# Optimization experiments

Hardware: AMD Instinct MI355X
Metric: run time of the kernel (lower is better)

Reference implementation:

```python
import jax, jax.numpy as jnp
import numpy as np

EMBED = 256
PC_RANGE = np.array([-51.2, -51.2, -5.0, 51.2, 51.2, 3.0], np.float32)
INF_PC_RANGE = np.array([0.0, -51.2, -5.0, 102.4, 51.2, 3.0], np.float32)
EPS = 1e-5
NUM_THINGS = 3
THRESHOLD = 0.05


def _inverse_sigmoid(x):
    # mmdet inverse_sigmoid with eps=1e-5
    x = jnp.clip(x, 0.0, 1.0)
    x1 = jnp.clip(x, EPS, None)
    x2 = jnp.clip(1.0 - x, EPS, None)
    return jnp.log(x1 / x2)


def _norm2lidar(locs, pc_range):
    lo = jnp.asarray(pc_range[:3])
    hi = jnp.asarray(pc_range[3:])
    return locs * (hi - lo) + lo


def _lidar2norm(locs, pc_range):
    lo = jnp.asarray(pc_range[:3])
    hi = jnp.asarray(pc_range[3:])
    return (locs - lo) / (hi - lo)


def _transform(pts, calib):
    # pts [..., 3]; homogeneous transform with calib [4,4]
    h = jnp.concatenate([pts, jnp.ones_like(pts[..., :1])], -1)
    return jnp.einsum('ij,...j->...i', calib, h)[..., :3]


def setup_inputs() -> dict:
    key = jax.random.key(0)
    ks = jax.random.split(key, 16)
    L, BS, NI, NV, C = 6, 1, 8192, 16384, 3
    # logits shifted positive so sigmoid > 0.05 for every (query, class):
    # matching torch's duplicate-index gather semantics).
    inf_cls = jnp.abs(jax.random.normal(ks[0], (L, BS, NI, C), jnp.float32)) + 0.2
    inp = {
        'inf_outputs_classes': inf_cls,
        'inf_outputs_coords': jax.random.uniform(ks[1], (L, BS, NI, 4), jnp.float32),
        'inf_query': jax.random.normal(ks[2], (BS, NI, EMBED), jnp.float32),
        'inf_query_pos': jax.random.normal(ks[3], (BS, NI, EMBED), jnp.float32),
        'inf_reference': jax.random.normal(ks[4], (BS, NI, 4), jnp.float32),
        'veh_outputs_classes': jax.random.normal(ks[5], (L, BS, NV, C), jnp.float32),
        'veh_outputs_coords': jax.random.uniform(ks[6], (L, BS, NV, 4), jnp.float32),
        'veh_query': jax.random.normal(ks[7], (BS, NV, EMBED), jnp.float32),
        'veh_query_pos': jax.random.normal(ks[8], (BS, NV, EMBED), jnp.float32),
        'veh_reference': jax.random.normal(ks[9], (BS, NV, 4), jnp.float32),
    }
    # valid rigid inf->veh calibration T; module computes calib = inv(veh2inf_rt[0].T)
    th = 0.3
    T = np.eye(4, dtype=np.float64)
    T[:3, :3] = [[np.cos(th), -np.sin(th), 0.0], [np.sin(th), np.cos(th), 0.0], [0.0, 0.0, 1.0]]
    T[:3, 3] = [10.0, 2.0, 0.5]
    inp['veh2inf_rt'] = jnp.asarray(np.linalg.inv(T).T, jnp.float32)[None]
    s = 0.05
    inp['W_align'] = jax.random.normal(ks[10], (EMBED + 9, EMBED), jnp.float32) * s
    inp['b_align'] = jax.random.normal(ks[11], (EMBED,), jnp.float32) * s
    inp['W_align_pos'] = jax.random.normal(ks[12], (EMBED + 9, EMBED), jnp.float32) * s
    inp['b_align_pos'] = jax.random.normal(ks[13], (EMBED,), jnp.float32) * s
    return inp


def reference(inf_outputs_classes, inf_outputs_coords, inf_query, inf_query_pos,
              inf_reference, veh_outputs_classes, veh_outputs_coords, veh_query,
              veh_query_pos, veh_reference, veh2inf_rt, W_align, b_align,
              W_align_pos, b_align_pos):
    # calibration goes through numpy in the original -> constant, non-differentiable
    calib = jnp.asarray(np.linalg.inv(np.asarray(veh2inf_rt[0], np.float64).T), jnp.float32)

    # ---- filter_inf_lanes: threshold on last-layer sigmoid scores ----
    cls_score = jax.nn.sigmoid(inf_outputs_classes[-1])            # [bs, N, C]
    indexes = jnp.nonzero(cls_score.reshape(-1) > THRESHOLD)[0]
    bbox_index = indexes // NUM_THINGS                              # duplicates kept

    inf_outputs_classes = inf_outputs_classes[:, :, bbox_index, :]
    inf_outputs_coords = inf_outputs_coords[:, :, bbox_index, :]
    inf_query = inf_query[:, bbox_index, :]
    inf_query_pos = inf_query_pos[:, bbox_index, :]
    inf_reference = inf_reference[:, bbox_index, :]

    # ---- reference points: inf norm -> inf lidar -> veh lidar -> veh norm ----
    ref3 = jnp.concatenate([inf_reference[..., :2],
                            jnp.zeros_like(inf_reference[..., :1])], -1)  # [bs,N,3]
    locs = jax.nn.sigmoid(ref3)                    # _norm2lidar inverse_sigmoid mode
    locs = _norm2lidar(locs, INF_PC_RANGE)
    locs = _transform(locs, calib)
    locs = _inverse_sigmoid(_lidar2norm(locs, PC_RANGE))
    inf_reference = inf_reference.at[..., :2].set(locs[..., :2])

    # ---- per-layer bbox centers: same transform in sigmoid space ----
    bb3 = jnp.concatenate([inf_outputs_coords[..., :2],
                           jnp.zeros_like(inf_outputs_coords[..., :1])], -1)  # [L,bs,N,3]
    bb3 = _norm2lidar(bb3, INF_PC_RANGE)
    bb3 = _transform(bb3, calib)
    bb3 = _lidar2norm(bb3, PC_RANGE)
    inf_outputs_coords = inf_outputs_coords.at[..., :2].set(bb3[..., :2])

    # ---- cross-agent query alignment with rotation conditioning ----
    r = calib[:3, :3].reshape(9)
    r_b = jnp.broadcast_to(r, inf_query.shape[:-1] + (9,))
    inf_query = jnp.concatenate([inf_query, r_b], -1) @ W_align + b_align
    inf_query_pos = jnp.concatenate([inf_query_pos, r_b], -1) @ W_align_pos + b_align_pos

    # ---- complement vehicle-side sets with aligned inf lanes ----
    outputs_classes = jnp.concatenate([veh_outputs_classes, inf_outputs_classes], axis=2)
    outputs_coords = jnp.concatenate([veh_outputs_coords, inf_outputs_coords], axis=2)
    query = jnp.concatenate([veh_query, inf_query], axis=1)
    query_pos = jnp.concatenate([veh_query_pos, inf_query_pos], axis=1)
    reference = jnp.concatenate([veh_reference, inf_reference], axis=1)
    return (outputs_classes, outputs_coords, query, query_pos, reference)
```

## Files before the change

### kernel.cpp

```cpp
#include <hip/hip_runtime.h>
#include <hip/hip_bf16.h>

#define EMBED 256
#define LL 6

typedef __attribute__((ext_vector_type(8))) __bf16 bf16x8;
typedef __attribute__((ext_vector_type(4))) float f32x4;

#define SEL_THR (-2.9444389791664403f)

__global__ __launch_bounds__(1024) void k_select_calib(
        const float* __restrict__ cls, int n,
        const float* __restrict__ rt, float* __restrict__ calib,
        int* __restrict__ bbox, int* __restrict__ cnt) {
    __shared__ int warpCnt[16];
    int tid = threadIdx.x;
    int wid = tid >> 6, lane = tid & 63;

    if (tid == 0) {
        double a[4][8];
        for (int i = 0; i < 4; ++i)
            for (int j = 0; j < 4; ++j) {
                a[i][j]     = (double)rt[j * 4 + i];
                a[i][4 + j] = (i == j) ? 1.0 : 0.0;
            }
        for (int c = 0; c < 4; ++c) {
            int p = c; double best = fabs(a[c][c]);
            for (int r = c + 1; r < 4; ++r) { double v = fabs(a[r][c]); if (v > best) { best = v; p = r; } }
            if (p != c) for (int j = 0; j < 8; ++j) { double t = a[c][j]; a[c][j] = a[p][j]; a[p][j] = t; }
            double inv = 1.0 / a[c][c];
            for (int j = 0; j < 8; ++j) a[c][j] *= inv;
            for (int r = 0; r < 4; ++r) if (r != c) {
                double f = a[r][c];
                for (int j = 0; j < 8; ++j) a[r][j] -= f * a[c][j];
            }
        }
        for (int i = 0; i < 4; ++i)
            for (int j = 0; j < 4; ++j) calib[i * 4 + j] = (float)a[i][4 + j];
    }

    int PT = ((n + 1023) / 1024 + 3) & ~3;
    int PT4 = PT >> 2;
    int start = tid * PT;

    float4 v[16];
#pragma unroll
    for (int j4 = 0; j4 < 16; ++j4) {
        if (j4 < PT4) {
            int s = start + j4 * 4;
            if (s + 4 <= n) {
                v[j4] = *(const float4*)&cls[s];
            } else {
                float4 t; t.x = t.y = t.z = t.w = -1e30f;
                if (s + 0 < n) t.x = cls[s + 0];
                if (s + 1 < n) t.y = cls[s + 1];
                if (s + 2 < n) t.z = cls[s + 2];
                if (s + 3 < n) t.w = cls[s + 3];
                v[j4] = t;
            }
        }
    }
    int c = 0;
#pragma unroll
    for (int j4 = 0; j4 < 16; ++j4) {
        if (j4 < PT4) {
            c += (v[j4].x > SEL_THR) + (v[j4].y > SEL_THR) +
                 (v[j4].z > SEL_THR) + (v[j4].w > SEL_THR);
        }
    }
    int incl = c;
#pragma unroll
    for (int off = 1; off < 64; off <<= 1) {
        int u = __shfl_up(incl, off, 64);
        if (lane >= off) incl += u;
    }
    if (lane == 63) warpCnt[wid] = incl;
    __syncthreads();
    int base = 0;
    for (int w2 = 0; w2 < wid; ++w2) base += warpCnt[w2];
    int pos = base + incl - c;

#pragma unroll
    for (int j4 = 0; j4 < 16; ++j4) {
        if (j4 < PT4) {
            int s = start + j4 * 4;
            if (s + 0 < n && v[j4].x > SEL_THR) bbox[pos++] = (s + 0) / 3;
            if (s + 1 < n && v[j4].y > SEL_THR) bbox[pos++] = (s + 1) / 3;
            if (s + 2 < n && v[j4].z > SEL_THR) bbox[pos++] = (s + 2) / 3;
            if (s + 3 < n && v[j4].w > SEL_THR) bbox[pos++] = (s + 3) / 3;
        }
    }
    if (tid == 0) {
        int tot = 0;
        for (int w2 = 0; w2 < 16; ++w2) tot += warpCnt[w2];
        *cnt = tot;
    }
}

__global__ __launch_bounds__(256) void k_prep(
        const float* __restrict__ W0, const float* __restrict__ W1,
        const float* __restrict__ b0, const float* __restrict__ b1,
        const float* __restrict__ calib,
        __bf16* __restrict__ Wt0, __bf16* __restrict__ Wt1,
        float* __restrict__ bvec0, float* __restrict__ bvec1) {
    int which = blockIdx.z;
    const float* W = which ? W1 : W0;
    __bf16* Wt     = which ? Wt1 : Wt0;
    int k0 = blockIdx.x * 64, c0 = blockIdx.y * 64;
    __shared__ float T[64][65];
    int tid = threadIdx.x;
#pragma unroll
    for (int i = 0; i < 16; ++i) {
        int idx = i * 256 + tid;
        int kk = idx >> 6, cc = idx & 63;
        T[kk][cc] = W[(size_t)(k0 + kk) * EMBED + c0 + cc];
    }
    __syncthreads();
#pragma unroll
    for (int i = 0; i < 16; ++i) {
        int idx = i * 256 + tid;
        int cc = idx >> 6, kk = idx & 63;
        Wt[(size_t)(c0 + cc) * EMBED + k0 + kk] = (__bf16)T[kk][cc];
    }
    if (blockIdx.x == 0 && blockIdx.y == 0) {
        const float* b = which ? b1 : b0;
        float* o       = which ? bvec1 : bvec0;
        float s = b[tid];
#pragma unroll
        for (int u = 0; u < 9; ++u) {
            float r = calib[(u / 3) * 4 + (u % 3)];
            s += r * W[(EMBED + u) * EMBED + tid];
        }
        o[tid] = s;
    }
}

struct Plan {
    const float* src[8];
    int start[9];
    int n4[5];
    int dstOff[8];
    int perLay4[2];
    int layStride[2];
    int K, NI, NV, N;
};

__device__ __forceinline__ float inv_sig(float v) {
    v = fminf(fmaxf(v, 0.0f), 1.0f);
    float x1 = fmaxf(v, 1e-5f);
    float x2 = fmaxf(1.0f - v, 1e-5f);
    return logf(x1 / x2);
}

__global__ __launch_bounds__(256) void k_fused(Plan P, const int* __restrict__ bbox,
                                               const float* __restrict__ calib,
                                               float* __restrict__ out) {
    int bx = blockIdx.x;
    int j = 0;
    while (bx >= P.start[j + 1]) ++j;
    int lb  = bx - P.start[j];
    int tid = threadIdx.x;

    if (j < 5) {
#pragma unroll
        for (int it = 0; it < 4; ++it) {
            int i4 = lb * 1024 + it * 256 + tid;
            if (i4 < P.n4[j]) {
                float4 v = *(const float4*)&P.src[j][(size_t)i4 * 4];
                size_t d;
                if (j < 2) {
                    int l = i4 / P.perLay4[j];
                    int r = i4 - l * P.perLay4[j];
                    d = (size_t)P.dstOff[j] + (size_t)l * P.layStride[j] + (size_t)r * 4;
                } else {
                    d = (size_t)P.dstOff[j] + (size_t)i4 * 4;
                }
                *(float4*)&out[d] = v;
            }
        }
        return;
    }

    int k = lb * 256 + tid;
    if (k >= P.K) return;
    int box = bbox[k]; box = max(0, min(box, P.NI - 1));

    if (j == 5) {
        const float* s0 = P.src[5];
#pragma unroll
        for (int l = 0; l < LL; ++l) {
            const float* s = s0 + ((size_t)l * P.NI + box) * 3;
            size_t d = (size_t)P.dstOff[5] + ((size_t)l * P.N + P.NV) * 3 + (size_t)k * 3;
            out[d + 0] = s[0]; out[d + 1] = s[1]; out[d + 2] = s[2];
        }
    } else if (j == 6) {
        float c00 = calib[0], c01 = calib[1], c03 = calib[3];
        float c10 = calib[4], c11 = calib[5], c13 = calib[7];
        float zx = calib[2] * -5.0f, zy = calib[6] * -5.0f;
#pragma unroll
        for (int l = 0; l < LL; ++l) {
            float4 s = *(const float4*)&P.src[6][((size_t)l * P.NI + box) * 4];
            float X = s.x * 102.4f;
            float Y = s.y * 102.4f - 51.2f;
            float tx = c00 * X + c01 * Y + zx + c03;
            float ty = c10 * X + c11 * Y + zy + c13;
            float4 v = make_float4((tx + 51.2f) * (1.0f / 102.4f),
                                   (ty + 51.2f) * (1.0f / 102.4f), s.z, s.w);
            *(float4*)&out[(size_t)P.dstOff[6] + ((size_t)l * P.N + P.NV + k) * 4] = v;
        }
    } else {
        float4 s = *(const float4*)&P.src[7][(size_t)box * 4];
        float sx = 1.0f / (1.0f + expf(-s.x));
        float sy = 1.0f / (1.0f + expf(-s.y));
        float X = sx * 102.4f;
        float Y = sy * 102.4f - 51.2f;
        float tx = calib[0] * X + calib[1] * Y + calib[2] * -1.0f + calib[3];
        float ty = calib[4] * X + calib[5] * Y + calib[6] * -1.0f + calib[7];
        float4 v = make_float4(inv_sig((tx + 51.2f) * (1.0f / 102.4f)),
                               inv_sig((ty + 51.2f) * (1.0f / 102.4f)), s.z, s.w);
        *(float4*)&out[(size_t)P.dstOff[7] + ((size_t)P.NV + k) * 4] = v;
    }
}

__device__ __forceinline__ bf16x8 cvt8(float4 f0, float4 f1) {
    bf16x8 r;
    r[0] = (__bf16)f0.x; r[1] = (__bf16)f0.y; r[2] = (__bf16)f0.z; r[3] = (__bf16)f0.w;
    r[4] = (__bf16)f1.x; r[5] = (__bf16)f1.y; r[6] = (__bf16)f1.z; r[7] = (__bf16)f1.w;
    return r;
}

__global__ __launch_bounds__(256) void k_gemm_mfma(
        const float* __restrict__ q0, const float* __restrict__ q1,
        const int* __restrict__ bbox,
        const __bf16* __restrict__ Wt0, const __bf16* __restrict__ Wt1,
        const float* __restrict__ bvec0, const float* __restrict__ bvec1,
        float* __restrict__ out, int NI, int K, int off0, int off1) {
    int which = blockIdx.y;
    const float* q    = which ? q1 : q0;
    const __bf16* Wt  = which ? Wt1 : Wt0;
    const float* bvec = which ? bvec1 : bvec0;
    int out_off       = which ? off1 : off0;

    int tid  = threadIdx.x;
    int w    = tid >> 6;
    int lane = tid & 63;
    int lo16 = lane & 15;
    int kg   = lane >> 4;

    int r0 = blockIdx.x * 64;

    const float* aptr[4];
#pragma unroll
    for (int t = 0; t < 4; ++t) {
        int row = r0 + 16 * t + lo16;
        int rc = min(row, K - 1);
        int box = bbox[rc]; box = max(0, min(box, NI - 1));
        aptr[t] = q + (size_t)box * EMBED + kg * 8;
    }
    const __bf16* bptr[4];
#pragma unroll
    for (int t = 0; t < 4; ++t) {
        int col = w * 64 + 16 * t + lo16;
        bptr[t] = Wt + (size_t)col * EMBED + kg * 8;
    }

    f32x4 acc[4][4];
#pragma unroll
    for (int ct = 0; ct < 4; ++ct) {
        float bv = bvec[w * 64 + 16 * ct + lo16];
#pragma unroll
        for (int rt = 0; rt < 4; ++rt) {
            acc[rt][ct][0] = bv; acc[rt][ct][1] = bv; acc[rt][ct][2] = bv; acc[rt][ct][3] = bv;
        }
    }

    for (int s = 0; s < 8; ++s) {
        bf16x8 a[4], b[4];
#pragma unroll
        for (int t = 0; t < 4; ++t) {
            float4 f0 = *(const float4*)(aptr[t] + s * 32);
            float4 f1 = *(const float4*)(aptr[t] + s * 32 + 4);
            a[t] = cvt8(f0, f1);
            b[t] = *(const bf16x8*)(bptr[t] + s * 32);
        }
#pragma unroll
        for (int rt = 0; rt < 4; ++rt)
#pragma unroll
            for (int ct = 0; ct < 4; ++ct)
                acc[rt][ct] = __builtin_amdgcn_mfma_f32_16x16x32_bf16(a[rt], b[ct], acc[rt][ct], 0, 0, 0);
    }

#pragma unroll
    for (int rt = 0; rt < 4; ++rt) {
#pragma unroll
        for (int reg = 0; reg < 4; ++reg) {
            int row = r0 + 16 * rt + kg * 4 + reg;
            if (row < K) {
#pragma unroll
                for (int ct = 0; ct < 4; ++ct) {
                    int col = w * 64 + 16 * ct + lo16;
                    out[out_off + (size_t)row * EMBED + col] = acc[rt][ct][reg];
                }
            }
        }
    }
}

extern "C" void kernel_launch(void* const* d_in, const int* in_sizes, int n_in,
                              void* d_out, int out_size, void* d_ws, size_t ws_size,
                              hipStream_t stream) {
    const float* inf_cls   = (const float*)d_in[0];
    const float* inf_coord = (const float*)d_in[1];
    const float* inf_q     = (const float*)d_in[2];
    const float* inf_qp    = (const float*)d_in[3];
    const float* inf_ref   = (const float*)d_in[4];
    const float* veh_cls   = (const float*)d_in[5];
    const float* veh_coord = (const float*)d_in[6];
    const float* veh_q     = (const float*)d_in[7];
    const float* veh_qp    = (const float*)d_in[8];
    const float* veh_ref   = (const float*)d_in[9];
    const float* rt        = (const float*)d_in[10];
    const float* W0        = (const float*)d_in[11];
    const float* b0        = (const float*)d_in[12];
    const float* W1        = (const float*)d_in[13];
    const float* b1        = (const float*)d_in[14];
    float* out = (float*)d_out;

    int NI = in_sizes[0] / (LL * 3);
    int NV = in_sizes[5] / (LL * 3);
    int N  = out_size / 558;
    int K  = N - NV;

    int off_cls   = 0;
    int off_coord = LL * N * 3;
    int off_q     = off_coord + LL * N * 4;
    int off_qp    = off_q + N * EMBED;
    int off_ref   = off_qp + N * EMBED;

    char* ws = (char*)d_ws;
    float* calib = (float*)(ws);
    float* bvec0 = (float*)(ws + 128);
    float* bvec1 = (float*)(ws + 1152);
    int*   cnt   = (int*)(ws + 2176);
    int*   bbox  = (int*)(ws + 2304);
    __bf16* Wt0  = (__bf16*)(ws + 131072);
    __bf16* Wt1  = (__bf16*)(ws + 262144);

    hipLaunchKernelGGL(k_select_calib, dim3(1), dim3(1024), 0, stream,
                       inf_cls + (size_t)(LL - 1) * NI * 3, NI * 3, rt, calib, bbox, cnt);
    hipLaunchKernelGGL(k_prep, dim3(4, 4, 2), dim3(256), 0, stream,
                       W0, W1, b0, b1, calib, Wt0, Wt1, bvec0, bvec1);
    {
        Plan P;
        P.src[0] = veh_cls;   P.src[1] = veh_coord; P.src[2] = veh_q;
        P.src[3] = veh_qp;    P.src[4] = veh_ref;
        P.src[5] = inf_cls;   P.src[6] = inf_coord; P.src[7] = inf_ref;
        P.n4[0] = LL * NV * 3 / 4;  P.n4[1] = LL * NV * 4 / 4;
        P.n4[2] = NV * EMBED / 4;   P.n4[3] = NV * EMBED / 4;  P.n4[4] = NV * 4 / 4;
        P.dstOff[0] = off_cls;   P.dstOff[1] = off_coord; P.dstOff[2] = off_q;
        P.dstOff[3] = off_qp;    P.dstOff[4] = off_ref;
        P.dstOff[5] = off_cls;   P.dstOff[6] = off_coord; P.dstOff[7] = off_ref;
        P.perLay4[0] = NV * 3 / 4;  P.perLay4[1] = NV * 4 / 4;
        P.layStride[0] = N * 3;     P.layStride[1] = N * 4;
        P.K = K; P.NI = NI; P.NV = NV; P.N = N;
        int nb[8];
        for (int j = 0; j < 5; ++j) nb[j] = (P.n4[j] + 1023) / 1024;
        int gblk = (K + 255) / 256;
        nb[5] = gblk; nb[6] = gblk; nb[7] = gblk;
        P.start[0] = 0;
        for (int j = 0; j < 8; ++j) P.start[j + 1] = P.start[j] + (nb[j] > 0 ? nb[j] : 0);
        if (K > 0 ? P.start[8] > 0 : P.start[5] > 0) {
            int totalBlocks = (K > 0) ? P.start[8] : P.start[5];
            hipLaunchKernelGGL(k_fused, dim3(totalBlocks), dim3(256), 0, stream,
                               P, bbox, calib, out);
        }
    }
    if (K > 0) {
        int gb = (K + 63) / 64;
        hipLaunchKernelGGL(k_gemm_mfma, dim3(gb, 2), dim3(256), 0, stream,
                           inf_q, inf_qp, bbox, Wt0, Wt1, bvec0, bvec1,
                           out, NI, K, off_q + NV * EMBED, off_qp + NV * EMBED);
    }
}
```

Baseline: 67.61 us.

## Merge four launches into two: fold weight prep into select, GEMM into copy kernel

```diff
diff --git a/kernel.cpp b/kernel.cpp
--- a/kernel.cpp
+++ b/kernel.cpp
@@ -9,12 +9,43 @@
 
 #define SEL_THR (-2.9444389791664403f)
 
-__global__ __launch_bounds__(1024) void k_select_calib(
+__global__ __launch_bounds__(1024) void k12(
         const float* __restrict__ cls, int n,
-        const float* __restrict__ rt, float* __restrict__ calib,
-        int* __restrict__ bbox, int* __restrict__ cnt) {
+        const float* __restrict__ rt,
+        const float* __restrict__ W0, const float* __restrict__ W1,
+        const float* __restrict__ b0, const float* __restrict__ b1,
+        float* __restrict__ calib,
+        int* __restrict__ bbox, int* __restrict__ cnt,
+        __bf16* __restrict__ Wt0, __bf16* __restrict__ Wt1,
+        float* __restrict__ bvec0, float* __restrict__ bvec1) {
+    int tid = threadIdx.x;
+
+    if (blockIdx.x != 0) {
+        int idx0 = blockIdx.x - 1;
+        int which = idx0 >> 4;
+        int t = idx0 & 15;
+        int k0 = (t >> 2) * 64, c0 = (t & 3) * 64;
+        const float* W = which ? W1 : W0;
+        __bf16* Wt     = which ? Wt1 : Wt0;
+        __shared__ float T[64][65];
+#pragma unroll
+        for (int i = 0; i < 4; ++i) {
+            int idx = i * 1024 + tid;
+            int kk = idx >> 6, cc = idx & 63;
+            T[kk][cc] = W[(size_t)(k0 + kk) * EMBED + c0 + cc];
+        }
+        __syncthreads();
+#pragma unroll
+        for (int i = 0; i < 4; ++i) {
+            int idx = i * 1024 + tid;
+            int cc = idx >> 6, kk = idx & 63;
+            Wt[(size_t)(c0 + cc) * EMBED + k0 + kk] = (__bf16)T[kk][cc];
+        }
+        return;
+    }
+
     __shared__ int warpCnt[16];
-    int tid = threadIdx.x;
+    __shared__ float s_calib[16];
     int wid = tid >> 6, lane = tid & 63;
 
     if (tid == 0) {
@@ -27,7 +58,7 @@
         for (int c = 0; c < 4; ++c) {
             int p = c; double best = fabs(a[c][c]);
             for (int r = c + 1; r < 4; ++r) { double v = fabs(a[r][c]); if (v > best) { best = v; p = r; } }
-            if (p != c) for (int j = 0; j < 8; ++j) { double t = a[c][j]; a[c][j] = a[p][j]; a[p][j] = t; }
+            if (p != c) for (int j = 0; j < 8; ++j) { double t2 = a[c][j]; a[c][j] = a[p][j]; a[p][j] = t2; }
             double inv = 1.0 / a[c][c];
             for (int j = 0; j < 8; ++j) a[c][j] *= inv;
             for (int r = 0; r < 4; ++r) if (r != c) {
@@ -36,7 +67,11 @@
             }
         }
         for (int i = 0; i < 4; ++i)
-            for (int j = 0; j < 4; ++j) calib[i * 4 + j] = (float)a[i][4 + j];
+            for (int j = 0; j < 4; ++j) {
+                float v = (float)a[i][4 + j];
+                calib[i * 4 + j] = v;
+                s_calib[i * 4 + j] = v;
+            }
     }
 
     int PT = ((n + 1023) / 1024 + 3) & ~3;
@@ -51,12 +86,12 @@
             if (s + 4 <= n) {
                 v[j4] = *(const float4*)&cls[s];
             } else {
-                float4 t; t.x = t.y = t.z = t.w = -1e30f;
-                if (s + 0 < n) t.x = cls[s + 0];
-                if (s + 1 < n) t.y = cls[s + 1];
-                if (s + 2 < n) t.z = cls[s + 2];
-                if (s + 3 < n) t.w = cls[s + 3];
-                v[j4] = t;
+                float4 t2; t2.x = t2.y = t2.z = t2.w = -1e30f;
+                if (s + 0 < n) t2.x = cls[s + 0];
+                if (s + 1 < n) t2.y = cls[s + 1];
+                if (s + 2 < n) t2.z = cls[s + 2];
+                if (s + 3 < n) t2.w = cls[s + 3];
+                v[j4] = t2;
             }
         }
     }
@@ -76,10 +111,10 @@
     }
     if (lane == 63) warpCnt[wid] = incl;
     __syncthreads();
+
     int base = 0;
     for (int w2 = 0; w2 < wid; ++w2) base += warpCnt[w2];
     int pos = base + incl - c;
-
 #pragma unroll
     for (int j4 = 0; j4 < 16; ++j4) {
         if (j4 < PT4) {
@@ -95,53 +130,36 @@
         for (int w2 = 0; w2 < 16; ++w2) tot += warpCnt[w2];
         *cnt = tot;
     }
-}
-
-__global__ __launch_bounds__(256) void k_prep(
-        const float* __restrict__ W0, const float* __restrict__ W1,
-        const float* __restrict__ b0, const float* __restrict__ b1,
-        const float* __restrict__ calib,
-        __bf16* __restrict__ Wt0, __bf16* __restrict__ Wt1,
-        float* __restrict__ bvec0, float* __restrict__ bvec1) {
-    int which = blockIdx.z;
-    const float* W = which ? W1 : W0;
-    __bf16* Wt     = which ? Wt1 : Wt0;
-    int k0 = blockIdx.x * 64, c0 = blockIdx.y * 64;
-    __shared__ float T[64][65];
-    int tid = threadIdx.x;
-#pragma unroll
-    for (int i = 0; i < 16; ++i) {
-        int idx = i * 256 + tid;
-        int kk = idx >> 6, cc = idx & 63;
-        T[kk][cc] = W[(size_t)(k0 + kk) * EMBED + c0 + cc];
-    }
-    __syncthreads();
-#pragma unroll
-    for (int i = 0; i < 16; ++i) {
-        int idx = i * 256 + tid;
-        int cc = idx >> 6, kk = idx & 63;
-        Wt[(size_t)(c0 + cc) * EMBED + k0 + kk] = (__bf16)T[kk][cc];
-    }
-    if (blockIdx.x == 0 && blockIdx.y == 0) {
+
+    if (tid < 512) {
+        int which = tid >> 8;
+        int j = tid & 255;
+        const float* W = which ? W1 : W0;
         const float* b = which ? b1 : b0;
         float* o       = which ? bvec1 : bvec0;
-        float s = b[tid];
+        float s = b[j];
 #pragma unroll
         for (int u = 0; u < 9; ++u) {
-            float r = calib[(u / 3) * 4 + (u % 3)];
-            s += r * W[(EMBED + u) * EMBED + tid];
-        }
-        o[tid] = s;
-    }
-}
-
-struct Plan {
-    const float* src[8];
-    int start[9];
+            float r = s_calib[(u / 3) * 4 + (u % 3)];
+            s += r * W[(EMBED + u) * EMBED + j];
+        }
+        o[j] = s;
+    }
+}
+
+struct Plan34 {
+    const float* vsrc[5];
+    const float* isrc[3];
+    const float* q0; const float* q1;
+    const __bf16* Wt0; const __bf16* Wt1;
+    const float* bvec0; const float* bvec1;
+    int start[11];
     int n4[5];
-    int dstOff[8];
+    int vdst[5];
+    int idst[3];
     int perLay4[2];
     int layStride[2];
+    int gemmOff0, gemmOff1;
     int K, NI, NV, N;
 };
 
@@ -152,28 +170,108 @@
     return logf(x1 / x2);
 }
 
-__global__ __launch_bounds__(256) void k_fused(Plan P, const int* __restrict__ bbox,
-                                               const float* __restrict__ calib,
-                                               float* __restrict__ out) {
+__device__ __forceinline__ bf16x8 cvt8(float4 f0, float4 f1) {
+    bf16x8 r;
+    r[0] = (__bf16)f0.x; r[1] = (__bf16)f0.y; r[2] = (__bf16)f0.z; r[3] = (__bf16)f0.w;
+    r[4] = (__bf16)f1.x; r[5] = (__bf16)f1.y; r[6] = (__bf16)f1.z; r[7] = (__bf16)f1.w;
+    return r;
+}
+
+__device__ void gemm_block(const float* __restrict__ q, const __bf16* __restrict__ Wt,
+                           const float* __restrict__ bvec, const int* __restrict__ bbox,
+                           float* __restrict__ out, int NI, int K, int out_off, int lb) {
+    int tid  = threadIdx.x;
+    int w    = tid >> 6;
+    int lane = tid & 63;
+    int lo16 = lane & 15;
+    int kg   = lane >> 4;
+    int r0 = lb * 64;
+
+    const float* aptr[4];
+#pragma unroll
+    for (int t = 0; t < 4; ++t) {
+        int row = r0 + 16 * t + lo16;
+        int rc = min(row, K - 1);
+        int box = bbox[rc]; box = max(0, min(box, NI - 1));
+        aptr[t] = q + (size_t)box * EMBED + kg * 8;
+    }
+    const __bf16* bptr[4];
+#pragma unroll
+    for (int t = 0; t < 4; ++t) {
+        int col = w * 64 + 16 * t + lo16;
+        bptr[t] = Wt + (size_t)col * EMBED + kg * 8;
+    }
+
+    f32x4 acc[4][4];
+#pragma unroll
+    for (int ct = 0; ct < 4; ++ct) {
+        float bv = bvec[w * 64 + 16 * ct + lo16];
+#pragma unroll
+        for (int rt = 0; rt < 4; ++rt) {
+            acc[rt][ct][0] = bv; acc[rt][ct][1] = bv; acc[rt][ct][2] = bv; acc[rt][ct][3] = bv;
+        }
+    }
+    for (int s = 0; s < 8; ++s) {
+        bf16x8 a[4], b[4];
+#pragma unroll
+        for (int t = 0; t < 4; ++t) {
+            float4 f0 = *(const float4*)(aptr[t] + s * 32);
+            float4 f1 = *(const float4*)(aptr[t] + s * 32 + 4);
+            a[t] = cvt8(f0, f1);
+            b[t] = *(const bf16x8*)(bptr[t] + s * 32);
+        }
+#pragma unroll
+        for (int rt = 0; rt < 4; ++rt)
+#pragma unroll
+            for (int ct = 0; ct < 4; ++ct)
+                acc[rt][ct] = __builtin_amdgcn_mfma_f32_16x16x32_bf16(a[rt], b[ct], acc[rt][ct], 0, 0, 0);
+    }
+#pragma unroll
+    for (int rt = 0; rt < 4; ++rt) {
+#pragma unroll
+        for (int reg = 0; reg < 4; ++reg) {
+            int row = r0 + 16 * rt + kg * 4 + reg;
+            if (row < K) {
+#pragma unroll
+                for (int ct = 0; ct < 4; ++ct) {
+                    int col = w * 64 + 16 * ct + lo16;
+                    out[out_off + (size_t)row * EMBED + col] = acc[rt][ct][reg];
+                }
+            }
+        }
+    }
+}
+
+__global__ __launch_bounds__(256) void k34(Plan34 P, const int* __restrict__ bbox,
+                                           const float* __restrict__ calib,
+                                           float* __restrict__ out) {
     int bx = blockIdx.x;
     int j = 0;
     while (bx >= P.start[j + 1]) ++j;
     int lb  = bx - P.start[j];
     int tid = threadIdx.x;
 
-    if (j < 5) {
+    if (j < 2) {
+        if (j == 0) gemm_block(P.q0, P.Wt0, P.bvec0, bbox, out, P.NI, P.K, P.gemmOff0, lb);
+        else        gemm_block(P.q1, P.Wt1, P.bvec1, bbox, out, P.NI, P.K, P.gemmOff1, lb);
+        return;
+    }
+
+    if (j < 7) {
+        const int cmap[5] = {2, 3, 0, 1, 4};
+        int cj = cmap[j - 2];
 #pragma unroll
         for (int it = 0; it < 4; ++it) {
             int i4 = lb * 1024 + it * 256 + tid;
-            if (i4 < P.n4[j]) {
-                float4 v = *(const float4*)&P.src[j][(size_t)i4 * 4];
+            if (i4 < P.n4[cj]) {
+                float4 v = *(const float4*)&P.vsrc[cj][(size_t)i4 * 4];
                 size_t d;
-                if (j < 2) {
-                    int l = i4 / P.perLay4[j];
-                    int r = i4 - l * P.perLay4[j];
-                    d = (size_t)P.dstOff[j] + (size_t)l * P.layStride[j] + (size_t)r * 4;
+                if (cj < 2) {
+                    int l = i4 / P.perLay4[cj];
+                    int r = i4 - l * P.perLay4[cj];
+                    d = (size_t)P.vdst[cj] + (size_t)l * P.layStride[cj] + (size_t)r * 4;
                 } else {
-                    d = (size_t)P.dstOff[j] + (size_t)i4 * 4;
+                    d = (size_t)P.vdst[cj] + (size_t)i4 * 4;
                 }
                 *(float4*)&out[d] = v;
             }
@@ -185,31 +283,31 @@
     if (k >= P.K) return;
     int box = bbox[k]; box = max(0, min(box, P.NI - 1));
 
-    if (j == 5) {
-        const float* s0 = P.src[5];
+    if (j == 7) {
+        const float* s0 = P.isrc[0];
 #pragma unroll
         for (int l = 0; l < LL; ++l) {
             const float* s = s0 + ((size_t)l * P.NI + box) * 3;
-            size_t d = (size_t)P.dstOff[5] + ((size_t)l * P.N + P.NV) * 3 + (size_t)k * 3;
+            size_t d = (size_t)P.idst[0] + ((size_t)l * P.N + P.NV) * 3 + (size_t)k * 3;
             out[d + 0] = s[0]; out[d + 1] = s[1]; out[d + 2] = s[2];
         }
-    } else if (j == 6) {
+    } else if (j == 8) {
         float c00 = calib[0], c01 = calib[1], c03 = calib[3];
         float c10 = calib[4], c11 = calib[5], c13 = calib[7];
         float zx = calib[2] * -5.0f, zy = calib[6] * -5.0f;
 #pragma unroll
         for (int l = 0; l < LL; ++l) {
-            float4 s = *(const float4*)&P.src[6][((size_t)l * P.NI + box) * 4];
+            float4 s = *(const float4*)&P.isrc[1][((size_t)l * P.NI + box) * 4];
             float X = s.x * 102.4f;
             float Y = s.y * 102.4f - 51.2f;
             float tx = c00 * X + c01 * Y + zx + c03;
             float ty = c10 * X + c11 * Y + zy + c13;
             float4 v = make_float4((tx + 51.2f) * (1.0f / 102.4f),
                                    (ty + 51.2f) * (1.0f / 102.4f), s.z, s.w);
-            *(float4*)&out[(size_t)P.dstOff[6] + ((size_t)l * P.N + P.NV + k) * 4] = v;
+            *(float4*)&out[(size_t)P.idst[1] + ((size_t)l * P.N + P.NV + k) * 4] = v;
         }
     } else {
-        float4 s = *(const float4*)&P.src[7][(size_t)box * 4];
+        float4 s = *(const float4*)&P.isrc[2][(size_t)box * 4];
         float sx = 1.0f / (1.0f + expf(-s.x));
         float sy = 1.0f / (1.0f + expf(-s.y));
         float X = sx * 102.4f;
@@ -218,91 +316,7 @@
         float ty = calib[4] * X + calib[5] * Y + calib[6] * -1.0f + calib[7];
         float4 v = make_float4(inv_sig((tx + 51.2f) * (1.0f / 102.4f)),
                                inv_sig((ty + 51.2f) * (1.0f / 102.4f)), s.z, s.w);
-        *(float4*)&out[(size_t)P.dstOff[7] + ((size_t)P.NV + k) * 4] = v;
-    }
-}
-
-__device__ __forceinline__ bf16x8 cvt8(float4 f0, float4 f1) {
-    bf16x8 r;
-    r[0] = (__bf16)f0.x; r[1] = (__bf16)f0.y; r[2] = (__bf16)f0.z; r[3] = (__bf16)f0.w;
-    r[4] = (__bf16)f1.x; r[5] = (__bf16)f1.y; r[6] = (__bf16)f1.z; r[7] = (__bf16)f1.w;
-    return r;
-}
-
-__global__ __launch_bounds__(256) void k_gemm_mfma(
-        const float* __restrict__ q0, const float* __restrict__ q1,
-        const int* __restrict__ bbox,
-        const __bf16* __restrict__ Wt0, const __bf16* __restrict__ Wt1,
-        const float* __restrict__ bvec0, const float* __restrict__ bvec1,
-        float* __restrict__ out, int NI, int K, int off0, int off1) {
-    int which = blockIdx.y;
-    const float* q    = which ? q1 : q0;
-    const __bf16* Wt  = which ? Wt1 : Wt0;
-    const float* bvec = which ? bvec1 : bvec0;
-    int out_off       = which ? off1 : off0;
-
-    int tid  = threadIdx.x;
-    int w    = tid >> 6;
-    int lane = tid & 63;
-    int lo16 = lane & 15;
-    int kg   = lane >> 4;
-
-    int r0 = blockIdx.x * 64;
-
-    const float* aptr[4];
-#pragma unroll
-    for (int t = 0; t < 4; ++t) {
-        int row = r0 + 16 * t + lo16;
-        int rc = min(row, K - 1);
-        int box = bbox[rc]; box = max(0, min(box, NI - 1));
-        aptr[t] = q + (size_t)box * EMBED + kg * 8;
-    }
-    const __bf16* bptr[4];
-#pragma unroll
-    for (int t = 0; t < 4; ++t) {
-        int col = w * 64 + 16 * t + lo16;
-        bptr[t] = Wt + (size_t)col * EMBED + kg * 8;
-    }
-
-    f32x4 acc[4][4];
-#pragma unroll
-    for (int ct = 0; ct < 4; ++ct) {
-        float bv = bvec[w * 64 + 16 * ct + lo16];
-#pragma unroll
-        for (int rt = 0; rt < 4; ++rt) {
-            acc[rt][ct][0] = bv; acc[rt][ct][1] = bv; acc[rt][ct][2] = bv; acc[rt][ct][3] = bv;
-        }
-    }
-
-    for (int s = 0; s < 8; ++s) {
-        bf16x8 a[4], b[4];
-#pragma unroll
-        for (int t = 0; t < 4; ++t) {
-            float4 f0 = *(const float4*)(aptr[t] + s * 32);
-            float4 f1 = *(const float4*)(aptr[t] + s * 32 + 4);
-            a[t] = cvt8(f0, f1);
-            b[t] = *(const bf16x8*)(bptr[t] + s * 32);
-        }
-#pragma unroll
-        for (int rt = 0; rt < 4; ++rt)
-#pragma unroll
-            for (int ct = 0; ct < 4; ++ct)
-                acc[rt][ct] = __builtin_amdgcn_mfma_f32_16x16x32_bf16(a[rt], b[ct], acc[rt][ct], 0, 0, 0);
-    }
-
-#pragma unroll
-    for (int rt = 0; rt < 4; ++rt) {
-#pragma unroll
-        for (int reg = 0; reg < 4; ++reg) {
-            int row = r0 + 16 * rt + kg * 4 + reg;
-            if (row < K) {
-#pragma unroll
-                for (int ct = 0; ct < 4; ++ct) {
-                    int col = w * 64 + 16 * ct + lo16;
-                    out[out_off + (size_t)row * EMBED + col] = acc[rt][ct][reg];
-                }
-            }
-        }
+        *(float4*)&out[(size_t)P.idst[2] + ((size_t)P.NV + k) * 4] = v;
     }
 }
 
@@ -346,39 +360,43 @@
     __bf16* Wt0  = (__bf16*)(ws + 131072);
     __bf16* Wt1  = (__bf16*)(ws + 262144);
 
-    hipLaunchKernelGGL(k_select_calib, dim3(1), dim3(1024), 0, stream,
-                       inf_cls + (size_t)(LL - 1) * NI * 3, NI * 3, rt, calib, bbox, cnt);
-    hipLaunchKernelGGL(k_prep, dim3(4, 4, 2), dim3(256), 0, stream,
-                       W0, W1, b0, b1, calib, Wt0, Wt1, bvec0, bvec1);
+    hipLaunchKernelGGL(k12, dim3(33), dim3(1024), 0, stream,
+                       inf_cls + (size_t)(LL - 1) * NI * 3, NI * 3, rt,
+                       W0, W1, b0, b1, calib, bbox, cnt, Wt0, Wt1, bvec0, bvec1);
+
     {
-        Plan P;
-        P.src[0] = veh_cls;   P.src[1] = veh_coord; P.src[2] = veh_q;
-        P.src[3] = veh_qp;    P.src[4] = veh_ref;
-        P.src[5] = inf_cls;   P.src[6] = inf_coord; P.src[7] = inf_ref;
+        Plan34 P;
+        P.vsrc[0] = veh_cls; P.vsrc[1] = veh_coord; P.vsrc[2] = veh_q;
+        P.vsrc[3] = veh_qp;  P.vsrc[4] = veh_ref;
+        P.isrc[0] = inf_cls; P.isrc[1] = inf_coord; P.isrc[2] = inf_ref;
+        P.q0 = inf_q; P.q1 = inf_qp;
+        P.Wt0 = Wt0; P.Wt1 = Wt1; P.bvec0 = bvec0; P.bvec1 = bvec1;
         P.n4[0] = LL * NV * 3 / 4;  P.n4[1] = LL * NV * 4 / 4;
         P.n4[2] = NV * EMBED / 4;   P.n4[3] = NV * EMBED / 4;  P.n4[4] = NV * 4 / 4;
-        P.dstOff[0] = off_cls;   P.dstOff[1] = off_coord; P.dstOff[2] = off_q;
-        P.dstOff[3] = off_qp;    P.dstOff[4] = off_ref;
-        P.dstOff[5] = off_cls;   P.dstOff[6] = off_coord; P.dstOff[7] = off_ref;
+        P.vdst[0] = off_cls; P.vdst[1] = off_coord; P.vdst[2] = off_q;
+        P.vdst[3] = off_qp;  P.vdst[4] = off_ref;
+        P.idst[0] = off_cls; P.idst[1] = off_coord; P.idst[2] = off_ref;
         P.perLay4[0] = NV * 3 / 4;  P.perLay4[1] = NV * 4 / 4;
         P.layStride[0] = N * 3;     P.layStride[1] = N * 4;
+        P.gemmOff0 = off_q + NV * EMBED;
+        P.gemmOff1 = off_qp + NV * EMBED;
         P.K = K; P.NI = NI; P.NV = NV; P.N = N;
-        int nb[8];
-        for (int j = 0; j < 5; ++j) nb[j] = (P.n4[j] + 1023) / 1024;
-        int gblk = (K + 255) / 256;
-        nb[5] = gblk; nb[6] = gblk; nb[7] = gblk;
+
+        int nbG = (K > 0) ? (K + 63) / 64 : 0;
+        int gblk = (K > 0) ? (K + 255) / 256 : 0;
+        int nb[10];
+        nb[0] = nbG; nb[1] = nbG;
+        nb[2] = (P.n4[2] + 1023) / 1024;
+        nb[3] = (P.n4[3] + 1023) / 1024;
+        nb[4] = (P.n4[0] + 1023) / 1024;
+        nb[5] = (P.n4[1] + 1023) / 1024;
+        nb[6] = (P.n4[4] + 1023) / 1024;
+        nb[7] = gblk; nb[8] = gblk; nb[9] = gblk;
         P.start[0] = 0;
-        for (int j = 0; j < 8; ++j) P.start[j + 1] = P.start[j] + (nb[j] > 0 ? nb[j] : 0);
-        if (K > 0 ? P.start[8] > 0 : P.start[5] > 0) {
-            int totalBlocks = (K > 0) ? P.start[8] : P.start[5];
-            hipLaunchKernelGGL(k_fused, dim3(totalBlocks), dim3(256), 0, stream,
+        for (int j = 0; j < 10; ++j) P.start[j + 1] = P.start[j] + nb[j];
+        if (P.start[10] > 0) {
+            hipLaunchKernelGGL(k34, dim3(P.start[10]), dim3(256), 0, stream,
                                P, bbox, calib, out);
         }
     }
-    if (K > 0) {
-        int gb = (K + 63) / 64;
-        hipLaunchKernelGGL(k_gemm_mfma, dim3(gb, 2), dim3(256), 0, stream,
-                           inf_q, inf_qp, bbox, Wt0, Wt1, bvec0, bvec1,
-                           out, NI, K, off_q + NV * EMBED, off_qp + NV * EMBED);
-    }
-}
+}
```

After: 100.2 us. 48.2% more time.
